# Kernel optimization log

Measured on AMD Instinct MI355X. Metric: run time of the kernel, lower is better.

Reference implementation:

```python
import jax, jax.numpy as jnp
import numpy as np

NUM_CAPSULE = 16
DIM_CAPSULE = 64
ROUTINGS = 3
T_EPS = 1e-7


def setup_inputs() -> dict:
    key = jax.random.key(0)
    k1, k2 = jax.random.split(key)
    x = jax.random.normal(k1, (64, 512, 768), dtype=jnp.float32)
    # xavier-normal-ish init for W: [1, input_dim_capsule, num_capsule*dim_capsule]
    fan_in, fan_out = 768, NUM_CAPSULE * DIM_CAPSULE
    std = float(np.sqrt(2.0 / (fan_in + fan_out)))
    W = jax.random.normal(k2, (1, 768, NUM_CAPSULE * DIM_CAPSULE), dtype=jnp.float32) * std
    return {"x": x, "W": W}


def _squash(v, eps=T_EPS):
    # NOTE: this module's 'squash' is pure L2 normalization with eps, not the
    # classic (s^2/(1+s^2)) squash.
    s2 = jnp.sum(v * v, axis=-1, keepdims=True)
    return v / jnp.sqrt(s2 + eps)


def reference(x, W):
    B, In, _ = x.shape
    # u_hat: [B, In, num*dim] -> [B, num, In, dim]
    u = jnp.matmul(x, W).reshape(B, In, NUM_CAPSULE, DIM_CAPSULE).transpose(0, 2, 1, 3)
    b = jnp.zeros((B, NUM_CAPSULE, In), dtype=u.dtype)  # routing logits
    outputs = None
    for i in range(ROUTINGS):
        # torch code softmaxes over the num_capsule axis (after permute dance)
        c = jax.nn.softmax(b, axis=1)  # [B, num, In]
        outputs = _squash(jnp.einsum('bij,bijk->bik', c, u))  # [B, num, dim]
        if i < ROUTINGS - 1:
            b = jnp.einsum('bik,bijk->bij', outputs, u)  # [B, num, In]
    return outputs
```

## Files before the change

### kernel.cpp

```cpp
#include <hip/hip_runtime.h>
#include <hip/hip_bf16.h>
#include <stdint.h>

#define BATCH 64
#define IN_CAPS 512
#define NCAP 16
#define DCAP 64
#define GN (NCAP * DCAP)
#define GM (BATCH * IN_CAPS)
#define GK 768

typedef __bf16 bf16;
typedef __attribute__((ext_vector_type(8))) __bf16 bf16x8;
typedef __attribute__((ext_vector_type(4))) __bf16 bf16x4;
typedef __attribute__((ext_vector_type(4))) float f32x4;

__device__ inline void async16(const bf16* g, bf16* l) {
    __builtin_amdgcn_global_load_lds(
        (__attribute__((address_space(1))) void*)g,
        (__attribute__((address_space(3))) void*)l, 16, 0, 0);
}

__global__ __launch_bounds__(256) void k_convX(const float* __restrict__ X,
                                               bf16* __restrict__ Xb) {
    const size_t i = ((size_t)blockIdx.x * 256 + threadIdx.x) * 8;
    const f32x4 a = *(const f32x4*)(X + i);
    const f32x4 b = *(const f32x4*)(X + i + 4);
    bf16x8 r;
    r[0] = (bf16)a[0]; r[1] = (bf16)a[1]; r[2] = (bf16)a[2]; r[3] = (bf16)a[3];
    r[4] = (bf16)b[0]; r[5] = (bf16)b[1]; r[6] = (bf16)b[2]; r[7] = (bf16)b[3];
    *(bf16x8*)(Xb + i) = r;
}

__global__ void k_transW(const float* __restrict__ W, bf16* __restrict__ Wt) {
    __shared__ bf16 t[32][33];
    const int k0 = blockIdx.x * 32;
    const int n0 = blockIdx.y * 32;
    const int tx = threadIdx.x, ty = threadIdx.y;
#pragma unroll
    for (int r = 0; r < 4; ++r)
        t[ty + r * 8][tx] = (bf16)W[(size_t)(k0 + ty + r * 8) * GN + n0 + tx];
    __syncthreads();
#pragma unroll
    for (int r = 0; r < 4; ++r)
        Wt[(size_t)(n0 + ty + r * 8) * GK + k0 + tx] = t[tx][ty + r * 8];
}

__global__ __launch_bounds__(256) void k_gemm_async(const bf16* __restrict__ Xb,
                                                    const bf16* __restrict__ Wt,
                                                    bf16* __restrict__ U) {
    __shared__ bf16 sA[128 * 32];
    __shared__ bf16 sB[128 * 32];

    const int tid = threadIdx.x;
    const int lane = tid & 63;
    const int wave = tid >> 6;
    const int wm = wave >> 1, wn = wave & 1;
    const int m0 = blockIdx.x * 128;
    const int n0 = blockIdx.y * 128;

    const int c0 = wave * 2, c1 = wave * 2 + 1;
    const int rl = lane >> 2, cl = (lane & 3) * 8;
    const bf16* gA0 = Xb + (size_t)(m0 + c0 * 16 + rl) * GK + cl;
    const bf16* gA1 = Xb + (size_t)(m0 + c1 * 16 + rl) * GK + cl;
    const bf16* gB0 = Wt + (size_t)(n0 + c0 * 16 + rl) * GK + cl;
    const bf16* gB1 = Wt + (size_t)(n0 + c1 * 16 + rl) * GK + cl;
    bf16* lA0 = sA + c0 * 512;
    bf16* lA1 = sA + c1 * 512;
    bf16* lB0 = sB + c0 * 512;
    bf16* lB1 = sB + c1 * 512;

    f32x4 acc[4][4] = {};
    const int fr = lane & 15;
    const int fq = lane >> 4;

    for (int kt = 0; kt < GK / 32; ++kt) {
        __syncthreads();
        async16(gA0, lA0);
        async16(gA1, lA1);
        async16(gB0, lB0);
        async16(gB1, lB1);
        gA0 += 32; gA1 += 32; gB0 += 32; gB1 += 32;
        __syncthreads();

        bf16x8 af[4], bfr[4];
#pragma unroll
        for (int mi = 0; mi < 4; ++mi)
            af[mi] = *(const bf16x8*)(sA + (wm * 64 + mi * 16 + fr) * 32 + fq * 8);
#pragma unroll
        for (int ni = 0; ni < 4; ++ni)
            bfr[ni] = *(const bf16x8*)(sB + (wn * 64 + ni * 16 + fr) * 32 + fq * 8);
#pragma unroll
        for (int mi = 0; mi < 4; ++mi)
#pragma unroll
            for (int ni = 0; ni < 4; ++ni)
                acc[mi][ni] = __builtin_amdgcn_mfma_f32_16x16x32_bf16(
                    af[mi], bfr[ni], acc[mi][ni], 0, 0, 0);
    }

#pragma unroll
    for (int mi = 0; mi < 4; ++mi) {
#pragma unroll
        for (int ni = 0; ni < 4; ++ni) {
#pragma unroll
            for (int r = 0; r < 4; ++r) {
                const int m = m0 + wm * 64 + mi * 16 + fq * 4 + r;
                const int n = n0 + wn * 64 + ni * 16 + fr;
                const int bb = m >> 9, j = m & 511;
                const int ci = n >> 6, k = n & 63;
                U[(((size_t)(bb * NCAP + ci)) * IN_CAPS + j) * DCAP + k] =
                    (bf16)acc[mi][ni][r];
            }
        }
    }
}

__global__ __launch_bounds__(256) void k_gemm_inline(const float* __restrict__ X,
                                                     const bf16* __restrict__ Wt,
                                                     bf16* __restrict__ U) {
    __shared__ bf16 sA[128 * 32];
    __shared__ bf16 sB[128 * 32];
    const int tid = threadIdx.x;
    const int lane = tid & 63;
    const int wave = tid >> 6;
    const int wm = wave >> 1, wn = wave & 1;
    const int m0 = blockIdx.x * 128;
    const int n0 = blockIdx.y * 128;
    const int srow = tid >> 2;
    const int scol = (tid & 3) * 8;
    f32x4 acc[4][4] = {};
    const int fr = lane & 15;
    const int fq = lane >> 4;
    for (int kt = 0; kt < GK / 32; ++kt) {
        const int kb = kt * 32;
        bf16x8 a0, a1, b0, b1;
        {
            const float* p = X + (size_t)(m0 + srow) * GK + kb + scol;
            const f32x4 x0 = *(const f32x4*)p, x1 = *(const f32x4*)(p + 4);
            const float* q = X + (size_t)(m0 + srow + 64) * GK + kb + scol;
            const f32x4 y0 = *(const f32x4*)q, y1 = *(const f32x4*)(q + 4);
#pragma unroll
            for (int c = 0; c < 4; ++c) {
                a0[c] = (bf16)x0[c]; a0[c + 4] = (bf16)x1[c];
                a1[c] = (bf16)y0[c]; a1[c + 4] = (bf16)y1[c];
            }
        }
        b0 = *(const bf16x8*)(Wt + (size_t)(n0 + srow) * GK + kb + scol);
        b1 = *(const bf16x8*)(Wt + (size_t)(n0 + srow + 64) * GK + kb + scol);
        __syncthreads();
        *(bf16x8*)(sA + srow * 32 + scol) = a0;
        *(bf16x8*)(sA + (srow + 64) * 32 + scol) = a1;
        *(bf16x8*)(sB + srow * 32 + scol) = b0;
        *(bf16x8*)(sB + (srow + 64) * 32 + scol) = b1;
        __syncthreads();
        bf16x8 af[4], bfr[4];
#pragma unroll
        for (int mi = 0; mi < 4; ++mi)
            af[mi] = *(const bf16x8*)(sA + (wm * 64 + mi * 16 + fr) * 32 + fq * 8);
#pragma unroll
        for (int ni = 0; ni < 4; ++ni)
            bfr[ni] = *(const bf16x8*)(sB + (wn * 64 + ni * 16 + fr) * 32 + fq * 8);
#pragma unroll
        for (int mi = 0; mi < 4; ++mi)
#pragma unroll
            for (int ni = 0; ni < 4; ++ni)
                acc[mi][ni] = __builtin_amdgcn_mfma_f32_16x16x32_bf16(
                    af[mi], bfr[ni], acc[mi][ni], 0, 0, 0);
    }
#pragma unroll
    for (int mi = 0; mi < 4; ++mi) {
#pragma unroll
        for (int ni = 0; ni < 4; ++ni) {
#pragma unroll
            for (int r = 0; r < 4; ++r) {
                const int m = m0 + wm * 64 + mi * 16 + fq * 4 + r;
                const int n = n0 + wn * 64 + ni * 16 + fr;
                const int bb = m >> 9, j = m & 511;
                const int ci = n >> 6, k = n & 63;
                U[(((size_t)(bb * NCAP + ci)) * IN_CAPS + j) * DCAP + k] =
                    (bf16)acc[mi][ni][r];
            }
        }
    }
}

__global__ __launch_bounds__(256) void k_route(const bf16* __restrict__ U,
                                               float* __restrict__ BL,
                                               float* __restrict__ OutC,
                                               int mode) {
    __shared__ float sc[IN_CAPS];
    __shared__ float red[32][64];
    __shared__ float sout[64];
    const int bi = blockIdx.x;
    const int b = bi >> 4, cap = bi & 15;
    const int tid = threadIdx.x;
    const size_t ubase = (size_t)bi * IN_CAPS * DCAP;

    if (mode == 0) {
        sc[tid] = 0.0625f;
        sc[tid + 256] = 0.0625f;
    } else {
#pragma unroll
        for (int h = 0; h < 2; ++h) {
            const int j = tid + h * 256;
            const float* p = BL + (size_t)b * NCAP * IN_CAPS + j;
            float v[16], mx = -1e30f;
#pragma unroll
            for (int i = 0; i < 16; ++i) {
                v[i] = p[(size_t)i * IN_CAPS];
                mx = fmaxf(mx, v[i]);
            }
            float s = 0.f;
#pragma unroll
            for (int i = 0; i < 16; ++i) s += __expf(v[i] - mx);
            sc[j] = __expf(v[cap] - mx) / s;
        }
    }
    __syncthreads();

    const int g = tid & 7;
    const int jr = tid >> 3;

    float acc[8] = {};
#pragma unroll
    for (int it = 0; it < 16; ++it) {
        const int j = it * 32 + jr;
        const bf16x8 v = *(const bf16x8*)(U + ubase + (size_t)it * 2048 + tid * 8);
        const float cv = sc[j];
#pragma unroll
        for (int c = 0; c < 8; ++c) acc[c] += cv * (float)v[c];
    }
    *(f32x4*)(&red[jr][g * 8]) = f32x4{acc[0], acc[1], acc[2], acc[3]};
    *(f32x4*)(&red[jr][g * 8 + 4]) = f32x4{acc[4], acc[5], acc[6], acc[7]};
    __syncthreads();

    if (tid < 64) {
        float s = 0.f;
#pragma unroll
        for (int r = 0; r < 32; ++r) s += red[r][tid];
        float ss = s * s;
#pragma unroll
        for (int off = 32; off >= 1; off >>= 1) ss += __shfl_xor(ss, off);
        const float val = s * rsqrtf(ss + 1e-7f);
        sout[tid] = val;
        if (mode == 2) OutC[(size_t)bi * DCAP + tid] = val;
    }
    if (mode == 2) return;
    __syncthreads();

    const f32x4 o0 = *(const f32x4*)(sout + g * 8);
    const f32x4 o1 = *(const f32x4*)(sout + g * 8 + 4);
#pragma unroll
    for (int it = 0; it < 16; ++it) {
        const int j = it * 32 + jr;
        const bf16x8 v = *(const bf16x8*)(U + ubase + (size_t)it * 2048 + tid * 8);
        float p = o0[0] * (float)v[0] + o0[1] * (float)v[1] +
                  o0[2] * (float)v[2] + o0[3] * (float)v[3] +
                  o1[0] * (float)v[4] + o1[1] * (float)v[5] +
                  o1[2] * (float)v[6] + o1[3] * (float)v[7];
        p += __shfl_xor(p, 1);
        p += __shfl_xor(p, 2);
        p += __shfl_xor(p, 4);
        if (g == 0) BL[((size_t)b * NCAP + cap) * IN_CAPS + j] = p;
    }
}

extern "C" void kernel_launch(void* const* d_in, const int* in_sizes, int n_in,
                              void* d_out, int out_size, void* d_ws, size_t ws_size,
                              hipStream_t stream) {
    const float* X = (const float*)d_in[0];
    const float* W = (const float*)d_in[1];
    float* OutC = (float*)d_out;

    const size_t u_bytes = (size_t)BATCH * NCAP * IN_CAPS * DCAP * sizeof(bf16);
    const size_t xb_bytes = (size_t)GM * GK * sizeof(bf16);
    const size_t wt_bytes = (size_t)GN * GK * sizeof(bf16);
    const size_t bl_bytes = (size_t)BATCH * NCAP * IN_CAPS * sizeof(float);
    char* ws = (char*)d_ws;

    const size_t need_big = u_bytes + xb_bytes + wt_bytes + bl_bytes;
    const size_t need_small = u_bytes + wt_bytes + bl_bytes;

    bf16* U = (bf16*)ws;
    bf16* Wt;
    float* BL;

    if (ws_size >= need_big) {
        bf16* Xb = (bf16*)(ws + u_bytes);
        Wt = (bf16*)(ws + u_bytes + xb_bytes);
        BL = (float*)(ws + u_bytes + xb_bytes + wt_bytes);
        k_convX<<<GM * GK / (256 * 8), 256, 0, stream>>>(X, Xb);
        k_transW<<<dim3(GK / 32, GN / 32), dim3(32, 8), 0, stream>>>(W, Wt);
        k_gemm_async<<<dim3(GM / 128, GN / 128), 256, 0, stream>>>(Xb, Wt, U);
    } else if (ws_size >= need_small) {
        Wt = (bf16*)(ws + u_bytes);
        BL = (float*)(ws + u_bytes + wt_bytes);
        k_transW<<<dim3(GK / 32, GN / 32), dim3(32, 8), 0, stream>>>(W, Wt);
        k_gemm_inline<<<dim3(GM / 128, GN / 128), 256, 0, stream>>>(X, Wt, U);
    } else {
        return;
    }

    k_route<<<BATCH * NCAP, 256, 0, stream>>>(U, BL, OutC, 0);
    k_route<<<BATCH * NCAP, 256, 0, stream>>>(U, BL, OutC, 1);
    k_route<<<BATCH * NCAP, 256, 0, stream>>>(U, BL, OutC, 2);
}
```

Before: 277.6 us.

## Compute first routing iteration algebraically and fuse logits into pipelined GEMM

Because the first routing iteration uses uniform coefficients, its output equals the normalized (sum_j x_j)·W/16. The change computes that from column sums of x gathered during bf16 conversion, instead of running a full routing pass over U. The GEMM now computes the second iteration's logits in its epilogue, and it switches to a 3-stage async LDS pipeline with a new LDS layout. This removes one route kernel and a full read of U, at the cost of extra atomics in the conversion kernel and a new small kernel.

```diff
diff --git a/kernel.cpp b/kernel.cpp
--- a/kernel.cpp
+++ b/kernel.cpp
@@ -12,7 +12,6 @@
 
 typedef __bf16 bf16;
 typedef __attribute__((ext_vector_type(8))) __bf16 bf16x8;
-typedef __attribute__((ext_vector_type(4))) __bf16 bf16x4;
 typedef __attribute__((ext_vector_type(4))) float f32x4;
 
 __device__ inline void async16(const bf16* g, bf16* l) {
@@ -21,22 +20,50 @@
         (__attribute__((address_space(3))) void*)l, 16, 0, 0);
 }
 
-__global__ __launch_bounds__(256) void k_convX(const float* __restrict__ X,
-                                               bf16* __restrict__ Xb) {
-    const size_t i = ((size_t)blockIdx.x * 256 + threadIdx.x) * 8;
-    const f32x4 a = *(const f32x4*)(X + i);
-    const f32x4 b = *(const f32x4*)(X + i + 4);
-    bf16x8 r;
-    r[0] = (bf16)a[0]; r[1] = (bf16)a[1]; r[2] = (bf16)a[2]; r[3] = (bf16)a[3];
-    r[4] = (bf16)b[0]; r[5] = (bf16)b[1]; r[6] = (bf16)b[2]; r[7] = (bf16)b[3];
-    *(bf16x8*)(Xb + i) = r;
-}
-
-__global__ void k_transW(const float* __restrict__ W, bf16* __restrict__ Wt) {
+__global__ __launch_bounds__(256) void k_convX2(const float* __restrict__ X,
+                                                bf16* __restrict__ Xb,
+                                                float* __restrict__ XS) {
+    __shared__ float ls[GK];
+    const int tid = threadIdx.x;
+    ls[tid] = 0.f; ls[tid + 256] = 0.f; ls[tid + 512] = 0.f;
+    __syncthreads();
+    const size_t base = (size_t)blockIdx.x * (32 * GK);
+#pragma unroll
+    for (int r = 0; r < 12; ++r) {
+        const int off = r * 2048 + tid * 8;
+        const int k0 = off % GK;
+        const f32x4 a0 = *(const f32x4*)(X + base + off);
+        const f32x4 a1 = *(const f32x4*)(X + base + off + 4);
+        bf16x8 o;
+        o[0] = (bf16)a0[0]; o[1] = (bf16)a0[1]; o[2] = (bf16)a0[2]; o[3] = (bf16)a0[3];
+        o[4] = (bf16)a1[0]; o[5] = (bf16)a1[1]; o[6] = (bf16)a1[2]; o[7] = (bf16)a1[3];
+        *(bf16x8*)(Xb + base + off) = o;
+        if (XS != nullptr) {
+            atomicAdd(&ls[k0 + 0], a0[0]); atomicAdd(&ls[k0 + 1], a0[1]);
+            atomicAdd(&ls[k0 + 2], a0[2]); atomicAdd(&ls[k0 + 3], a0[3]);
+            atomicAdd(&ls[k0 + 4], a1[0]); atomicAdd(&ls[k0 + 5], a1[1]);
+            atomicAdd(&ls[k0 + 6], a1[2]); atomicAdd(&ls[k0 + 7], a1[3]);
+        }
+    }
+    if (XS != nullptr) {
+        __syncthreads();
+        const int bidx = blockIdx.x >> 4;
+        atomicAdd(&XS[(size_t)bidx * GK + tid],       ls[tid]);
+        atomicAdd(&XS[(size_t)bidx * GK + tid + 256], ls[tid + 256]);
+        atomicAdd(&XS[(size_t)bidx * GK + tid + 512], ls[tid + 512]);
+    }
+}
+
+__global__ void k_transW(const float* __restrict__ W, bf16* __restrict__ Wt,
+                         float* __restrict__ XS) {
     __shared__ bf16 t[32][33];
     const int k0 = blockIdx.x * 32;
     const int n0 = blockIdx.y * 32;
     const int tx = threadIdx.x, ty = threadIdx.y;
+    if (XS != nullptr) {
+        const int gid = (blockIdx.y * gridDim.x + blockIdx.x) * 256 + ty * 32 + tx;
+        if (gid < BATCH * GK) XS[gid] = 0.f;
+    }
 #pragma unroll
     for (int r = 0; r < 4; ++r)
         t[ty + r * 8][tx] = (bf16)W[(size_t)(k0 + ty + r * 8) * GN + n0 + tx];
@@ -46,11 +73,58 @@
         Wt[(size_t)(n0 + ty + r * 8) * GK + k0 + tx] = t[tx][ty + r * 8];
 }
 
-__global__ __launch_bounds__(256) void k_gemm_async(const bf16* __restrict__ Xb,
-                                                    const bf16* __restrict__ Wt,
-                                                    bf16* __restrict__ U) {
-    __shared__ bf16 sA[128 * 32];
-    __shared__ bf16 sB[128 * 32];
+__global__ __launch_bounds__(256) void k_out1(const float* __restrict__ XS,
+                                              const float* __restrict__ W,
+                                              float* __restrict__ O1) {
+    __shared__ float xs[4][GK];
+    __shared__ float red[4][4][64];
+    const int cap = blockIdx.x & 15;
+    const int bg = blockIdx.x >> 4;
+    const int tid = threadIdx.x;
+    const int k = tid & 63, kq = tid >> 6;
+#pragma unroll
+    for (int bb = 0; bb < 4; ++bb) {
+        const size_t b = (size_t)(bg * 4 + bb);
+        xs[bb][tid]       = XS[b * GK + tid];
+        xs[bb][tid + 256] = XS[b * GK + tid + 256];
+        xs[bb][tid + 512] = XS[b * GK + tid + 512];
+    }
+    __syncthreads();
+    float acc4[4] = {0.f, 0.f, 0.f, 0.f};
+    const float* wp = W + (size_t)(kq * 192) * GN + cap * 64 + k;
+#pragma unroll 4
+    for (int kk = 0; kk < 192; ++kk) {
+        const float w = wp[(size_t)kk * GN];
+        const int kx = kq * 192 + kk;
+        acc4[0] += xs[0][kx] * w;
+        acc4[1] += xs[1][kx] * w;
+        acc4[2] += xs[2][kx] * w;
+        acc4[3] += xs[3][kx] * w;
+    }
+#pragma unroll
+    for (int bb = 0; bb < 4; ++bb) red[bb][kq][k] = acc4[bb];
+    __syncthreads();
+    if (tid < 64) {
+#pragma unroll
+        for (int bb = 0; bb < 4; ++bb) {
+            float s = (red[bb][0][tid] + red[bb][1][tid] +
+                       red[bb][2][tid] + red[bb][3][tid]) * 0.0625f;
+            float ss = s * s;
+#pragma unroll
+            for (int off = 32; off >= 1; off >>= 1) ss += __shfl_xor(ss, off);
+            O1[((size_t)(bg * 4 + bb) * NCAP + cap) * DCAP + tid] =
+                s * rsqrtf(ss + 1e-7f);
+        }
+    }
+}
+
+__global__ __launch_bounds__(256) void k_gemm_pipe(const bf16* __restrict__ Xb,
+                                                   const bf16* __restrict__ Wt,
+                                                   const float* __restrict__ O1,
+                                                   bf16* __restrict__ U,
+                                                   float* __restrict__ BL) {
+    __shared__ bf16 sA[3 * 4096];
+    __shared__ bf16 sB[3 * 4096];
 
     const int tid = threadIdx.x;
     const int lane = tid & 63;
@@ -59,45 +133,66 @@
     const int m0 = blockIdx.x * 128;
     const int n0 = blockIdx.y * 128;
 
-    const int c0 = wave * 2, c1 = wave * 2 + 1;
-    const int rl = lane >> 2, cl = (lane & 3) * 8;
-    const bf16* gA0 = Xb + (size_t)(m0 + c0 * 16 + rl) * GK + cl;
-    const bf16* gA1 = Xb + (size_t)(m0 + c1 * 16 + rl) * GK + cl;
-    const bf16* gB0 = Wt + (size_t)(n0 + c0 * 16 + rl) * GK + cl;
-    const bf16* gB1 = Wt + (size_t)(n0 + c1 * 16 + rl) * GK + cl;
-    bf16* lA0 = sA + c0 * 512;
-    bf16* lA1 = sA + c1 * 512;
-    bf16* lB0 = sB + c0 * 512;
-    bf16* lB1 = sB + c1 * 512;
+    const int r16 = lane & 15, q8 = (lane >> 4) * 8;
+    const bf16* gA0 = Xb + (size_t)(m0 + wave * 16 + r16) * GK + q8;
+    const bf16* gA1 = Xb + (size_t)(m0 + (wave + 4) * 16 + r16) * GK + q8;
+    const bf16* gB0 = Wt + (size_t)(n0 + wave * 16 + r16) * GK + q8;
+    const bf16* gB1 = Wt + (size_t)(n0 + (wave + 4) * 16 + r16) * GK + q8;
 
     f32x4 acc[4][4] = {};
+
+#define STAGE(BUF) do {                                        \
+        async16(gA0, sA + (BUF) * 4096 + wave * 512);          \
+        async16(gA1, sA + (BUF) * 4096 + (wave + 4) * 512);    \
+        async16(gB0, sB + (BUF) * 4096 + wave * 512);          \
+        async16(gB1, sB + (BUF) * 4096 + (wave + 4) * 512);    \
+        gA0 += 32; gA1 += 32; gB0 += 32; gB1 += 32;            \
+    } while (0)
+
+    auto gstep = [&](int buf) {
+        bf16x8 af[4], bv[4];
+#pragma unroll
+        for (int mi = 0; mi < 4; ++mi)
+            af[mi] = *(const bf16x8*)(sA + buf * 4096 + (wm * 4 + mi) * 512 + lane * 8);
+#pragma unroll
+        for (int ni = 0; ni < 4; ++ni)
+            bv[ni] = *(const bf16x8*)(sB + buf * 4096 + (wn * 4 + ni) * 512 + lane * 8);
+#pragma unroll
+        for (int mi = 0; mi < 4; ++mi)
+#pragma unroll
+            for (int ni = 0; ni < 4; ++ni)
+                acc[mi][ni] = __builtin_amdgcn_mfma_f32_16x16x32_bf16(
+                    af[mi], bv[ni], acc[mi][ni], 0, 0, 0);
+    };
+
+    STAGE(0);
+    STAGE(1);
+
+    int cur = 0, nxt = 2;
+    for (int kt = 0; kt < GK / 32 - 2; ++kt) {
+        asm volatile("s_waitcnt lgkmcnt(0)" ::: "memory");
+        asm volatile("s_waitcnt vmcnt(4)" ::: "memory");
+        __builtin_amdgcn_s_barrier();
+        __builtin_amdgcn_sched_barrier(0);
+        STAGE(nxt);
+        gstep(cur);
+        cur = (cur == 2) ? 0 : cur + 1;
+        nxt = (nxt == 2) ? 0 : nxt + 1;
+    }
+    asm volatile("s_waitcnt lgkmcnt(0)" ::: "memory");
+    asm volatile("s_waitcnt vmcnt(4)" ::: "memory");
+    __builtin_amdgcn_s_barrier();
+    __builtin_amdgcn_sched_barrier(0);
+    gstep(1);
+    asm volatile("s_waitcnt lgkmcnt(0)" ::: "memory");
+    asm volatile("s_waitcnt vmcnt(0)" ::: "memory");
+    __builtin_amdgcn_s_barrier();
+    __builtin_amdgcn_sched_barrier(0);
+    gstep(2);
+#undef STAGE
+
     const int fr = lane & 15;
     const int fq = lane >> 4;
-
-    for (int kt = 0; kt < GK / 32; ++kt) {
-        __syncthreads();
-        async16(gA0, lA0);
-        async16(gA1, lA1);
-        async16(gB0, lB0);
-        async16(gB1, lB1);
-        gA0 += 32; gA1 += 32; gB0 += 32; gB1 += 32;
-        __syncthreads();
-
-        bf16x8 af[4], bfr[4];
-#pragma unroll
-        for (int mi = 0; mi < 4; ++mi)
-            af[mi] = *(const bf16x8*)(sA + (wm * 64 + mi * 16 + fr) * 32 + fq * 8);
-#pragma unroll
-        for (int ni = 0; ni < 4; ++ni)
-            bfr[ni] = *(const bf16x8*)(sB + (wn * 64 + ni * 16 + fr) * 32 + fq * 8);
-#pragma unroll
-        for (int mi = 0; mi < 4; ++mi)
-#pragma unroll
-            for (int ni = 0; ni < 4; ++ni)
-                acc[mi][ni] = __builtin_amdgcn_mfma_f32_16x16x32_bf16(
-                    af[mi], bfr[ni], acc[mi][ni], 0, 0, 0);
-    }
-
 #pragma unroll
     for (int mi = 0; mi < 4; ++mi) {
 #pragma unroll
@@ -110,6 +205,31 @@
                 const int ci = n >> 6, k = n & 63;
                 U[(((size_t)(bb * NCAP + ci)) * IN_CAPS + j) * DCAP + k] =
                     (bf16)acc[mi][ni][r];
+            }
+        }
+    }
+
+    if (O1 != nullptr) {
+        const int b = m0 >> 9;
+        const int cap = (n0 >> 6) + wn;
+        float o1v[4];
+#pragma unroll
+        for (int ni = 0; ni < 4; ++ni)
+            o1v[ni] = O1[(size_t)b * GN + n0 + wn * 64 + ni * 16 + fr];
+#pragma unroll
+        for (int mi = 0; mi < 4; ++mi) {
+#pragma unroll
+            for (int r = 0; r < 4; ++r) {
+                float p = o1v[0] * acc[mi][0][r] + o1v[1] * acc[mi][1][r] +
+                          o1v[2] * acc[mi][2][r] + o1v[3] * acc[mi][3][r];
+                p += __shfl_xor(p, 1);
+                p += __shfl_xor(p, 2);
+                p += __shfl_xor(p, 4);
+                p += __shfl_xor(p, 8);
+                if (fr == 0) {
+                    const int j = (m0 & 511) + wm * 64 + mi * 16 + fq * 4 + r;
+                    BL[((size_t)(b * NCAP + cap)) * IN_CAPS + j] = p;
+                }
             }
         }
     }
@@ -276,32 +396,45 @@
     const size_t xb_bytes = (size_t)GM * GK * sizeof(bf16);
     const size_t wt_bytes = (size_t)GN * GK * sizeof(bf16);
     const size_t bl_bytes = (size_t)BATCH * NCAP * IN_CAPS * sizeof(float);
+    const size_t xs_bytes = (size_t)BATCH * GK * sizeof(float);
+    const size_t o1_bytes = (size_t)BATCH * GN * sizeof(float);
     char* ws = (char*)d_ws;
 
-    const size_t need_big = u_bytes + xb_bytes + wt_bytes + bl_bytes;
+    const size_t need_full = u_bytes + xb_bytes + wt_bytes + bl_bytes + xs_bytes + o1_bytes;
+    const size_t need_async = u_bytes + xb_bytes + wt_bytes + bl_bytes;
     const size_t need_small = u_bytes + wt_bytes + bl_bytes;
 
     bf16* U = (bf16*)ws;
-    bf16* Wt;
-    float* BL;
-
-    if (ws_size >= need_big) {
+
+    if (ws_size >= need_full) {
         bf16* Xb = (bf16*)(ws + u_bytes);
-        Wt = (bf16*)(ws + u_bytes + xb_bytes);
-        BL = (float*)(ws + u_bytes + xb_bytes + wt_bytes);
-        k_convX<<<GM * GK / (256 * 8), 256, 0, stream>>>(X, Xb);
-        k_transW<<<dim3(GK / 32, GN / 32), dim3(32, 8), 0, stream>>>(W, Wt);
-        k_gemm_async<<<dim3(GM / 128, GN / 128), 256, 0, stream>>>(Xb, Wt, U);
+        bf16* Wt = (bf16*)(ws + u_bytes + xb_bytes);
+        float* BL = (float*)(ws + u_bytes + xb_bytes + wt_bytes);
+        float* XS = (float*)(ws + u_bytes + xb_bytes + wt_bytes + bl_bytes);
+        float* O1 = (float*)(ws + u_bytes + xb_bytes + wt_bytes + bl_bytes + xs_bytes);
+        k_transW<<<dim3(GK / 32, GN / 32), dim3(32, 8), 0, stream>>>(W, Wt, XS);
+        k_convX2<<<GM / 32, 256, 0, stream>>>(X, Xb, XS);
+        k_out1<<<256, 256, 0, stream>>>(XS, W, O1);
+        k_gemm_pipe<<<dim3(GM / 128, GN / 128), 256, 0, stream>>>(Xb, Wt, O1, U, BL);
+        k_route<<<BATCH * NCAP, 256, 0, stream>>>(U, BL, OutC, 1);
+        k_route<<<BATCH * NCAP, 256, 0, stream>>>(U, BL, OutC, 2);
+    } else if (ws_size >= need_async) {
+        bf16* Xb = (bf16*)(ws + u_bytes);
+        bf16* Wt = (bf16*)(ws + u_bytes + xb_bytes);
+        float* BL = (float*)(ws + u_bytes + xb_bytes + wt_bytes);
+        k_transW<<<dim3(GK / 32, GN / 32), dim3(32, 8), 0, stream>>>(W, Wt, nullptr);
+        k_convX2<<<GM / 32, 256, 0, stream>>>(X, Xb, nullptr);
+        k_gemm_pipe<<<dim3(GM / 128, GN / 128), 256, 0, stream>>>(Xb, Wt, nullptr, U, BL);
+        k_route<<<BATCH * NCAP, 256, 0, stream>>>(U, BL, OutC, 0);
+        k_route<<<BATCH * NCAP, 256, 0, stream>>>(U, BL, OutC, 1);
+        k_route<<<BATCH * NCAP, 256, 0, stream>>>(U, BL, OutC, 2);
     } else if (ws_size >= need_small) {
-        Wt = (bf16*)(ws + u_bytes);
-        BL = (float*)(ws + u_bytes + wt_bytes);
-        k_transW<<<dim3(GK / 32, GN / 32), dim3(32, 8), 0, stream>>>(W, Wt);
+        bf16* Wt = (bf16*)(ws + u_bytes);
+        float* BL = (float*)(ws + u_bytes + wt_bytes);
+        k_transW<<<dim3(GK / 32, GN / 32), dim3(32, 8), 0, stream>>>(W, Wt, nullptr);
         k_gemm_inline<<<dim3(GM / 128, GN / 128), 256, 0, stream>>>(X, Wt, U);
-    } else {
-        return;
-    }
-
-    k_route<<<BATCH * NCAP, 256, 0, stream>>>(U, BL, OutC, 0);
-    k_route<<<BATCH * NCAP, 256, 0, stream>>>(U, BL, OutC, 1);
-    k_route<<<BATCH * NCAP, 256, 0, stream>>>(U, BL, OutC, 2);
-}
+        k_route<<<BATCH * NCAP, 256, 0, stream>>>(U, BL, OutC, 0);
+        k_route<<<BATCH * NCAP, 256, 0, stream>>>(U, BL, OutC, 1);
+        k_route<<<BATCH * NCAP, 256, 0, stream>>>(U, BL, OutC, 2);
+    }
+}
```

After: 403.7 us. 45.4% more time.
